# Kernel tuning notes

Hardware: AMD Instinct MI355X
Metric: run time of the kernel (lower is better)

Reference implementation:

```python
import jax, jax.numpy as jnp
import numpy as np

B, S, D = 8, 2048, 512
LN_EPS = 1e-5

def _layernorm(x, gamma, beta):
    mu = jnp.mean(x, axis=-1, keepdims=True)
    var = jnp.mean(jnp.square(x - mu), axis=-1, keepdims=True)
    return (x - mu) * jax.lax.rsqrt(var + LN_EPS) * gamma + beta

def setup_inputs() -> dict:
    key = jax.random.key(0)
    ks = jax.random.split(key, 10)
    s_in = 1.0 / np.sqrt(2 * D)
    s_d = 1.0 / np.sqrt(D)
    return {
        "Noise_x": jax.random.normal(ks[0], (B, S, D), jnp.float32),
        "X": jax.random.normal(ks[1], (B, S, D), jnp.float32),
        "cond": jax.random.normal(ks[2], (B, S, D), jnp.float32),
        "W_gate": jax.random.normal(ks[3], (2 * D, D), jnp.float32) * s_in,
        "b_gate": jnp.zeros((D,), jnp.float32),
        "W1": jax.random.normal(ks[4], (D, 2 * D), jnp.float32) * s_d,
        "b1": jnp.zeros((2 * D,), jnp.float32),
        "W2": jax.random.normal(ks[5], (2 * D, D), jnp.float32) * s_in,
        "b2": jnp.zeros((D,), jnp.float32),
        "g1": jnp.ones((D,), jnp.float32),
        "be1": jnp.zeros((D,), jnp.float32),
        "g2": jnp.ones((D,), jnp.float32),
        "be2": jnp.zeros((D,), jnp.float32),
    }

def reference(Noise_x, X, cond, W_gate, b_gate, W1, b1, W2, b2, g1, be1, g2, be2):
    # gated fusion of noise and condition
    combined = jnp.concatenate([Noise_x, cond], axis=-1)            # [B,S,2D]
    gate = jax.nn.sigmoid(combined @ W_gate + b_gate)               # [B,S,D]
    fused = gate * Noise_x + (1.0 - gate) * cond                    # [B,S,D]
    # hand-rolled attention: Q = fused, K = V = X
    scale = 1.0 / jnp.sqrt(jnp.asarray(D, fused.dtype))
    scores = jnp.einsum('bqd,bkd->bqk', fused, X) * scale           # [B,S,S]
    attn = jax.nn.softmax(scores, axis=-1)
    attn_out = jnp.einsum('bqk,bkd->bqd', attn, X)                  # [B,S,D]
    # residual + norm, FFN (exact GELU as in torch default), residual + norm
    q = _layernorm(fused + attn_out, g1, be1)
    ff = jax.nn.gelu(q @ W1 + b1, approximate=False) @ W2 + b2
    return _layernorm(q + ff, g2, be2)
```

## Files before the change

kernel.cpp:

```cpp
#include <hip/hip_runtime.h>
#include <math.h>

typedef unsigned short ushort_t;
typedef unsigned int uint_t;
typedef __attribute__((ext_vector_type(8))) short short8;
typedef __attribute__((ext_vector_type(4))) float floatx4;

constexpr int B = 8;
constexpr int S = 2048;
constexpr int D = 512;
constexpr int BS = B * S;
constexpr float LN_EPS = 1e-5f;
constexpr float ATTN_SCALE = 0.04419417382415922f;


__device__ __forceinline__ ushort_t f2bf(float f) {
    union { float f; uint_t u; } x; x.f = f;
    uint_t r = x.u + 0x7fffu + ((x.u >> 16) & 1u);
    return (ushort_t)(r >> 16);
}
__device__ __forceinline__ float bf2f(ushort_t h) {
    union { uint_t u; float f; } y; y.u = ((uint_t)h) << 16;
    return y.f;
}
__device__ __forceinline__ short8 pack8(float4 a, float4 b) {
    short8 p;
    p[0] = (short)f2bf(a.x); p[1] = (short)f2bf(a.y);
    p[2] = (short)f2bf(a.z); p[3] = (short)f2bf(a.w);
    p[4] = (short)f2bf(b.x); p[5] = (short)f2bf(b.y);
    p[6] = (short)f2bf(b.z); p[7] = (short)f2bf(b.w);
    return p;
}

__device__ __forceinline__ float blk_reduce_sum(float v, float* sm) {
#pragma unroll
    for (int o = 32; o; o >>= 1) v += __shfl_down(v, o, 64);
    __syncthreads();
    if ((threadIdx.x & 63) == 0) sm[threadIdx.x >> 6] = v;
    __syncthreads();
    return sm[0] + sm[1] + sm[2] + sm[3];
}
__device__ __forceinline__ float blk_reduce_max(float v, float* sm) {
#pragma unroll
    for (int o = 32; o; o >>= 1) v = fmaxf(v, __shfl_down(v, o, 64));
    __syncthreads();
    if ((threadIdx.x & 63) == 0) sm[threadIdx.x >> 6] = v;
    __syncthreads();
    return fmaxf(fmaxf(sm[0], sm[1]), fmaxf(sm[2], sm[3]));
}

__global__ __launch_bounds__(256) void transpose_cvt(
    const float* __restrict__ in, ushort_t* __restrict__ out, int R, int C) {
    __shared__ float tl[32][33];
    const size_t zoff = (size_t)blockIdx.z * R * C;
    const int tx = threadIdx.x & 31, ty = threadIdx.x >> 5;
    const int c0 = blockIdx.x * 32, r0 = blockIdx.y * 32;
#pragma unroll
    for (int i = 0; i < 4; i++)
        tl[ty + i * 8][tx] = in[zoff + (size_t)(r0 + ty + i * 8) * C + c0 + tx];
    __syncthreads();
#pragma unroll
    for (int i = 0; i < 4; i++)
        out[zoff + (size_t)(c0 + ty + i * 8) * R + r0 + tx] = f2bf(tl[tx][ty + i * 8]);
}

#define GEMM_PREAMBLE()                                                        \
    __shared__ ushort_t As[128 * 40];                                          \
    __shared__ ushort_t Bs[128 * 40];                                          \
    const int t = threadIdx.x;                                                 \
    const int m0 = blockIdx.y * 128, n0 = blockIdx.x * 128;                    \
    const int sr = t >> 2;                                          \
    const int sc = (t & 3) * 8;                                 \
    const int lane = t & 63, w = t >> 6;                                       \
    const int wm = (w >> 1) * 64, wn = (w & 1) * 64;                           \
    const int fr = lane & 15, fq = lane >> 4;                                  \
    floatx4 acc[4][4];                                                         \
    _Pragma("unroll") for (int i = 0; i < 4; i++)                              \
        _Pragma("unroll") for (int j = 0; j < 4; j++) {                        \
            acc[i][j][0] = 0.f; acc[i][j][1] = 0.f;                            \
            acc[i][j][2] = 0.f; acc[i][j][3] = 0.f; }

#define GEMM_MFMA_STAGE()                                                      \
    short8 af[4], bfg[4];                                                      \
    _Pragma("unroll") for (int i = 0; i < 4; i++) {                            \
        af[i]  = *(const short8*)&As[(wm + i * 16 + fr) * 40 + fq * 8];        \
        bfg[i] = *(const short8*)&Bs[(wn + i * 16 + fr) * 40 + fq * 8];        \
    }                                                                          \
    _Pragma("unroll") for (int i = 0; i < 4; i++)                              \
        _Pragma("unroll") for (int j = 0; j < 4; j++)                          \
            acc[i][j] = __builtin_amdgcn_mfma_f32_16x16x32_bf16(               \
                af[i], bfg[j], acc[i][j], 0, 0, 0);

__global__ __launch_bounds__(256) void gate_gemm(
    const float* __restrict__ NX, const float* __restrict__ CD,
    const ushort_t* __restrict__ WgT, const float* __restrict__ bg,
    ushort_t* __restrict__ Fb) {
    GEMM_PREAMBLE();
    const ushort_t* Bb = WgT + (size_t)n0 * 1024;

    for (int k0 = 0; k0 < 1024; k0 += 32) {
        const float* Asrc = (k0 < 512) ? NX : CD;
        const int kk = k0 & 511;
        const float* p0 = Asrc + (size_t)(m0 + sr) * 512 + kk + sc;
        const float* p1 = Asrc + (size_t)(m0 + sr + 64) * 512 + kk + sc;
        float4 f00 = *(const float4*)p0;       float4 f01 = *(const float4*)(p0 + 4);
        float4 f10 = *(const float4*)p1;       float4 f11 = *(const float4*)(p1 + 4);
        int4 b0 = *(const int4*)(Bb + (size_t)sr * 1024 + k0 + sc);
        int4 b1 = *(const int4*)(Bb + (size_t)(sr + 64) * 1024 + k0 + sc);
        short8 pa0 = pack8(f00, f01), pa1 = pack8(f10, f11);
        __syncthreads();
        *(short8*)&As[sr * 40 + sc] = pa0;
        *(short8*)&As[(sr + 64) * 40 + sc] = pa1;
        *(int4*)&Bs[sr * 40 + sc] = b0;
        *(int4*)&Bs[(sr + 64) * 40 + sc] = b1;
        __syncthreads();
        GEMM_MFMA_STAGE();
    }

#pragma unroll
    for (int i = 0; i < 4; i++) {
#pragma unroll
        for (int j = 0; j < 4; j++) {
#pragma unroll
            for (int r = 0; r < 4; r++) {
                const int m = m0 + wm + i * 16 + fq * 4 + r;
                const int n = n0 + wn + j * 16 + fr;
                const float z = acc[i][j][r] + bg[n];
                const float g = 1.f / (1.f + expf(-z));
                const size_t idx = (size_t)m * 512 + n;
                Fb[idx] = f2bf(g * NX[idx] + (1.f - g) * CD[idx]);
            }
        }
    }
}

#define GEMM3_PREAMBLE()                                                       \
    __shared__ ushort_t As[128 * 40];                                          \
    __shared__ ushort_t Bs[64 * 40];                                           \
    const int t = threadIdx.x;                                                 \
    const int m0 = blockIdx.y * 128, n0 = blockIdx.x * 64;                     \
    const int sr = t >> 2;                                          \
    const int sc = (t & 3) * 8;                                 \
    const int lane = t & 63, w = t >> 6;                                       \
    const int wm = w * 32;                                                     \
    const int fr = lane & 15, fq = lane >> 4;                                  \
    floatx4 acc[2][4];                                                         \
    _Pragma("unroll") for (int i = 0; i < 2; i++)                              \
        _Pragma("unroll") for (int j = 0; j < 4; j++) {                        \
            acc[i][j][0] = 0.f; acc[i][j][1] = 0.f;                            \
            acc[i][j][2] = 0.f; acc[i][j][3] = 0.f; }

#define GEMM3_MFMA_STAGE()                                                     \
    short8 af[2], bfg[4];                                                      \
    _Pragma("unroll") for (int i = 0; i < 2; i++)                              \
        af[i]  = *(const short8*)&As[(wm + i * 16 + fr) * 40 + fq * 8];        \
    _Pragma("unroll") for (int j = 0; j < 4; j++)                              \
        bfg[j] = *(const short8*)&Bs[(j * 16 + fr) * 40 + fq * 8];             \
    _Pragma("unroll") for (int i = 0; i < 2; i++)                              \
        _Pragma("unroll") for (int j = 0; j < 4; j++)                          \
            acc[i][j] = __builtin_amdgcn_mfma_f32_16x16x32_bf16(               \
                af[i], bfg[j], acc[i][j], 0, 0, 0);

template <int EPI>
__global__ __launch_bounds__(256) void gemm3_std(
    const ushort_t* __restrict__ A, int lda, long sAz,
    const ushort_t* __restrict__ Bt, int ldb, long sBz,
    void* __restrict__ Cv, int ldc, long sCz,
    int K, const float* __restrict__ bias, float scale, int init) {
    GEMM3_PREAMBLE();
    const ushort_t* Ab = A + (size_t)blockIdx.z * sAz + (size_t)m0 * lda;
    const ushort_t* Bb = Bt + (size_t)blockIdx.z * sBz + (size_t)n0 * ldb;

    for (int k0 = 0; k0 < K; k0 += 32) {
        int4 a0 = *(const int4*)(Ab + (size_t)sr * lda + k0 + sc);
        int4 a1 = *(const int4*)(Ab + (size_t)(sr + 64) * lda + k0 + sc);
        int4 b0 = *(const int4*)(Bb + (size_t)sr * ldb + k0 + sc);
        __syncthreads();
        *(int4*)&As[sr * 40 + sc] = a0;
        *(int4*)&As[(sr + 64) * 40 + sc] = a1;
        *(int4*)&Bs[sr * 40 + sc] = b0;
        __syncthreads();
        GEMM3_MFMA_STAGE();
    }

#pragma unroll
    for (int i = 0; i < 2; i++) {
#pragma unroll
        for (int j = 0; j < 4; j++) {
#pragma unroll
            for (int r = 0; r < 4; r++) {
                const int m = m0 + wm + i * 16 + fq * 4 + r;
                const int n = n0 + j * 16 + fr;
                float v = acc[i][j][r];
                if (EPI == 0) {
                    ushort_t* C = (ushort_t*)Cv + (size_t)blockIdx.z * sCz;
                    C[(size_t)m * ldc + n] = f2bf(v * scale);
                } else if (EPI == 1) {
                    const float x = v + bias[n];
                    const float gl = 0.5f * x * (1.f + erff(x * 0.70710678118654752f));
                    ushort_t* C = (ushort_t*)Cv;
                    C[(size_t)m * ldc + n] = f2bf(gl);
                } else {
                    float* T = (float*)Cv;
                    const size_t idx = (size_t)m * ldc + n;
                    T[idx] = T[idx] + v + (init ? bias[n] : 0.f);
                }
            }
        }
    }
}

__global__ __launch_bounds__(256) void qk_gemm3(
    const ushort_t* __restrict__ Qb, const float* __restrict__ Xf,
    ushort_t* __restrict__ Sc) {
    GEMM3_PREAMBLE();
    const ushort_t* Ab = Qb + (size_t)blockIdx.z * S * D + (size_t)m0 * D;
    const float*    Bf = Xf + (size_t)blockIdx.z * S * D + (size_t)n0 * D;
    ushort_t* Scb = Sc + (size_t)blockIdx.z * S * S;

    for (int k0 = 0; k0 < D; k0 += 32) {
        int4 a0 = *(const int4*)(Ab + (size_t)sr * D + k0 + sc);
        int4 a1 = *(const int4*)(Ab + (size_t)(sr + 64) * D + k0 + sc);
        const float* p0 = Bf + (size_t)sr * D + k0 + sc;
        float4 f00 = *(const float4*)p0;       float4 f01 = *(const float4*)(p0 + 4);
        short8 pb0 = pack8(f00, f01);
        __syncthreads();
        *(int4*)&As[sr * 40 + sc] = a0;
        *(int4*)&As[(sr + 64) * 40 + sc] = a1;
        *(short8*)&Bs[sr * 40 + sc] = pb0;
        __syncthreads();
        GEMM3_MFMA_STAGE();
    }

#pragma unroll
    for (int i = 0; i < 2; i++) {
#pragma unroll
        for (int j = 0; j < 4; j++) {
#pragma unroll
            for (int r = 0; r < 4; r++) {
                const int m = m0 + wm + i * 16 + fq * 4 + r;
                const int n = n0 + j * 16 + fr;
                Scb[(size_t)m * S + n] = f2bf(acc[i][j][r] * ATTN_SCALE);
            }
        }
    }
}

__global__ __launch_bounds__(256) void softmax_bf16(ushort_t* __restrict__ Sc) {
    __shared__ float sm[4];
    ushort_t* row = Sc + (size_t)blockIdx.x * 2048;
    const int t = threadIdx.x;
    ushort_t raw[8];
    *(int4*)raw = *(const int4*)(row + t * 8);
    float e[8];
    float mx = -1e30f;
#pragma unroll
    for (int j = 0; j < 8; j++) { e[j] = bf2f(raw[j]); mx = fmaxf(mx, e[j]); }
    mx = blk_reduce_max(mx, sm);
    float s = 0.f;
#pragma unroll
    for (int j = 0; j < 8; j++) { e[j] = expf(e[j] - mx); s += e[j]; }
    s = blk_reduce_sum(s, sm);
    const float inv = 1.f / s;
#pragma unroll
    for (int j = 0; j < 8; j++) raw[j] = f2bf(e[j] * inv);
    *(int4*)(row + t * 8) = *(const int4*)raw;
}

__global__ __launch_bounds__(256) void ln1_kernel(
    const ushort_t* __restrict__ Fb, const ushort_t* __restrict__ Ab,
    const float* __restrict__ g1, const float* __restrict__ be1,
    float* __restrict__ qf, ushort_t* __restrict__ qb) {
    __shared__ float sm[4];
    const size_t base = (size_t)blockIdx.x * 512;
    const int t = threadIdx.x;
    const float v0 = bf2f(Fb[base + t]) + bf2f(Ab[base + t]);
    const float v1 = bf2f(Fb[base + t + 256]) + bf2f(Ab[base + t + 256]);
    const float mu = blk_reduce_sum(v0 + v1, sm) * (1.f / 512.f);
    const float d0 = v0 - mu, d1 = v1 - mu;
    const float var = blk_reduce_sum(d0 * d0 + d1 * d1, sm) * (1.f / 512.f);
    const float rs = rsqrtf(var + LN_EPS);
    const float y0 = d0 * rs * g1[t] + be1[t];
    const float y1 = d1 * rs * g1[t + 256] + be1[t + 256];
    qf[base + t] = y0;          qf[base + t + 256] = y1;
    qb[base + t] = f2bf(y0);    qb[base + t + 256] = f2bf(y1);
}

__global__ __launch_bounds__(256) void ln2_kernel(
    float* __restrict__ T, const float* __restrict__ g,
    const float* __restrict__ be) {
    __shared__ float sm[4];
    const size_t base = (size_t)blockIdx.x * 512;
    const int t = threadIdx.x;
    const float v0 = T[base + t];
    const float v1 = T[base + t + 256];
    const float mu = blk_reduce_sum(v0 + v1, sm) * (1.f / 512.f);
    const float d0 = v0 - mu, d1 = v1 - mu;
    const float var = blk_reduce_sum(d0 * d0 + d1 * d1, sm) * (1.f / 512.f);
    const float rs = rsqrtf(var + LN_EPS);
    T[base + t] = d0 * rs * g[t] + be[t];
    T[base + t + 256] = d1 * rs * g[t + 256] + be[t + 256];
}

extern "C" void kernel_launch(void* const* d_in, const int* in_sizes, int n_in,
                              void* d_out, int out_size, void* d_ws, size_t ws_size,
                              hipStream_t stream) {
    const float* NX  = (const float*)d_in[0];
    const float* X   = (const float*)d_in[1];
    const float* CD  = (const float*)d_in[2];
    const float* Wg  = (const float*)d_in[3];
    const float* bg  = (const float*)d_in[4];
    const float* W1  = (const float*)d_in[5];
    const float* b1  = (const float*)d_in[6];
    const float* W2  = (const float*)d_in[7];
    const float* b2  = (const float*)d_in[8];
    const float* g1  = (const float*)d_in[9];
    const float* be1 = (const float*)d_in[10];
    const float* g2  = (const float*)d_in[11];
    const float* be2 = (const float*)d_in[12];

    ushort_t* slot0 = (ushort_t*)d_ws;
    ushort_t* slot1 = (ushort_t*)((char*)d_ws + 16777216);
    ushort_t* slot2 = (ushort_t*)((char*)d_ws + 33554432);
    ushort_t* attnb = slot0;
    ushort_t* hbuf  = slot0;
    ushort_t* Fb    = slot1;
    ushort_t* W1T   = slot1;
    ushort_t* W2T   = slot1 + 524288;
    ushort_t* WgT   = slot2;
    ushort_t* XbT   = slot2;
    ushort_t* qb    = slot2;
    ushort_t* Scb   = (ushort_t*)d_out;
    float*    qf    = (float*)d_out;

    transpose_cvt<<<dim3(512 / 32, 1024 / 32, 1), 256, 0, stream>>>(Wg, WgT, 1024, 512);

    gate_gemm<<<dim3(4, 128), 256, 0, stream>>>(NX, CD, WgT, bg, Fb);

    transpose_cvt<<<dim3(512 / 32, 2048 / 32, 8), 256, 0, stream>>>(X, XbT, 2048, 512);

    for (int g = 0; g < 2; g++) {
        const size_t go = (size_t)g * 4 * S * 512;
        qk_gemm3<<<dim3(32, 16, 4), 256, 0, stream>>>(Fb + go, X + go, Scb);
        softmax_bf16<<<4 * S, 256, 0, stream>>>(Scb);
        gemm3_std<0><<<dim3(8, 16, 4), 256, 0, stream>>>(
            Scb, S, (long)S * S,
            XbT + go, S, (long)D * S,
            (void*)(attnb + go), 512, (long)S * 512, S, nullptr, 1.f, 0);
    }

    ln1_kernel<<<BS, 256, 0, stream>>>(Fb, attnb, g1, be1, qf, qb);

    transpose_cvt<<<dim3(1024 / 32, 512 / 32, 1), 256, 0, stream>>>(W1, W1T, 512, 1024);
    transpose_cvt<<<dim3(512 / 32, 1024 / 32, 1), 256, 0, stream>>>(W2, W2T, 1024, 512);

    for (int h = 0; h < 2; h++) {
        gemm3_std<1><<<dim3(8, 128), 256, 0, stream>>>(
            qb, 512, 0, W1T + (size_t)h * 512 * 512, 512, 0,
            (void*)hbuf, 512, 0, 512, b1 + h * 512, 1.f, 0);
        gemm3_std<2><<<dim3(8, 128), 256, 0, stream>>>(
            hbuf, 512, 0, W2T + h * 512, 1024, 0,
            (void*)qf, 512, 0, 512, b2, 1.f, h == 0 ? 1 : 0);
    }

    ln2_kernel<<<BS, 256, 0, stream>>>(qf, g2, be2);
}
```

Measured before the change: 557.8 us.

## Prefetch next K-tile into registers during MFMA in all GEMM kernels

Each GEMM loop (generic, QK, gate) now loads the next K-slice from global memory into registers after the shared-memory store and before the MFMA stage, so global latency overlaps with compute. The gate GEMM also moves from a 128x128 tile to a 128x64 tile, doubling its grid. This is meant to hide global-load latency behind the MFMAs. In exchange it uses more live registers, and the smaller gate tile gives less data reuse per block.

Result: slower. 573.8 us (+2.9%).

```diff
diff --git a/kernel.cpp b/kernel.cpp
--- a/kernel.cpp
+++ b/kernel.cpp
@@ -62,76 +62,6 @@
 #pragma unroll
     for (int i = 0; i < 4; i++)
         out[zoff + (size_t)(c0 + ty + i * 8) * R + r0 + tx] = f2bf(tl[tx][ty + i * 8]);
-}
-
-#define GEMM_PREAMBLE()                                                        \
-    __shared__ ushort_t As[128 * 40];                                          \
-    __shared__ ushort_t Bs[128 * 40];                                          \
-    const int t = threadIdx.x;                                                 \
-    const int m0 = blockIdx.y * 128, n0 = blockIdx.x * 128;                    \
-    const int sr = t >> 2;                                          \
-    const int sc = (t & 3) * 8;                                 \
-    const int lane = t & 63, w = t >> 6;                                       \
-    const int wm = (w >> 1) * 64, wn = (w & 1) * 64;                           \
-    const int fr = lane & 15, fq = lane >> 4;                                  \
-    floatx4 acc[4][4];                                                         \
-    _Pragma("unroll") for (int i = 0; i < 4; i++)                              \
-        _Pragma("unroll") for (int j = 0; j < 4; j++) {                        \
-            acc[i][j][0] = 0.f; acc[i][j][1] = 0.f;                            \
-            acc[i][j][2] = 0.f; acc[i][j][3] = 0.f; }
-
-#define GEMM_MFMA_STAGE()                                                      \
-    short8 af[4], bfg[4];                                                      \
-    _Pragma("unroll") for (int i = 0; i < 4; i++) {                            \
-        af[i]  = *(const short8*)&As[(wm + i * 16 + fr) * 40 + fq * 8];        \
-        bfg[i] = *(const short8*)&Bs[(wn + i * 16 + fr) * 40 + fq * 8];        \
-    }                                                                          \
-    _Pragma("unroll") for (int i = 0; i < 4; i++)                              \
-        _Pragma("unroll") for (int j = 0; j < 4; j++)                          \
-            acc[i][j] = __builtin_amdgcn_mfma_f32_16x16x32_bf16(               \
-                af[i], bfg[j], acc[i][j], 0, 0, 0);
-
-__global__ __launch_bounds__(256) void gate_gemm(
-    const float* __restrict__ NX, const float* __restrict__ CD,
-    const ushort_t* __restrict__ WgT, const float* __restrict__ bg,
-    ushort_t* __restrict__ Fb) {
-    GEMM_PREAMBLE();
-    const ushort_t* Bb = WgT + (size_t)n0 * 1024;
-
-    for (int k0 = 0; k0 < 1024; k0 += 32) {
-        const float* Asrc = (k0 < 512) ? NX : CD;
-        const int kk = k0 & 511;
-        const float* p0 = Asrc + (size_t)(m0 + sr) * 512 + kk + sc;
-        const float* p1 = Asrc + (size_t)(m0 + sr + 64) * 512 + kk + sc;
-        float4 f00 = *(const float4*)p0;       float4 f01 = *(const float4*)(p0 + 4);
-        float4 f10 = *(const float4*)p1;       float4 f11 = *(const float4*)(p1 + 4);
-        int4 b0 = *(const int4*)(Bb + (size_t)sr * 1024 + k0 + sc);
-        int4 b1 = *(const int4*)(Bb + (size_t)(sr + 64) * 1024 + k0 + sc);
-        short8 pa0 = pack8(f00, f01), pa1 = pack8(f10, f11);
-        __syncthreads();
-        *(short8*)&As[sr * 40 + sc] = pa0;
-        *(short8*)&As[(sr + 64) * 40 + sc] = pa1;
-        *(int4*)&Bs[sr * 40 + sc] = b0;
-        *(int4*)&Bs[(sr + 64) * 40 + sc] = b1;
-        __syncthreads();
-        GEMM_MFMA_STAGE();
-    }
-
-#pragma unroll
-    for (int i = 0; i < 4; i++) {
-#pragma unroll
-        for (int j = 0; j < 4; j++) {
-#pragma unroll
-            for (int r = 0; r < 4; r++) {
-                const int m = m0 + wm + i * 16 + fq * 4 + r;
-                const int n = n0 + wn + j * 16 + fr;
-                const float z = acc[i][j][r] + bg[n];
-                const float g = 1.f / (1.f + expf(-z));
-                const size_t idx = (size_t)m * 512 + n;
-                Fb[idx] = f2bf(g * NX[idx] + (1.f - g) * CD[idx]);
-            }
-        }
-    }
 }
 
 #define GEMM3_PREAMBLE()                                                       \
@@ -151,18 +81,20 @@
             acc[i][j][2] = 0.f; acc[i][j][3] = 0.f; }
 
 #define GEMM3_MFMA_STAGE()                                                     \
-    short8 af[2], bfg[4];                                                      \
-    _Pragma("unroll") for (int i = 0; i < 2; i++)                              \
-        af[i]  = *(const short8*)&As[(wm + i * 16 + fr) * 40 + fq * 8];        \
-    _Pragma("unroll") for (int j = 0; j < 4; j++)                              \
-        bfg[j] = *(const short8*)&Bs[(j * 16 + fr) * 40 + fq * 8];             \
-    _Pragma("unroll") for (int i = 0; i < 2; i++)                              \
+    {                                                                          \
+        short8 af[2], bfg[4];                                                  \
+        _Pragma("unroll") for (int i = 0; i < 2; i++)                          \
+            af[i]  = *(const short8*)&As[(wm + i * 16 + fr) * 40 + fq * 8];    \
         _Pragma("unroll") for (int j = 0; j < 4; j++)                          \
-            acc[i][j] = __builtin_amdgcn_mfma_f32_16x16x32_bf16(               \
-                af[i], bfg[j], acc[i][j], 0, 0, 0);
+            bfg[j] = *(const short8*)&Bs[(j * 16 + fr) * 40 + fq * 8];         \
+        _Pragma("unroll") for (int i = 0; i < 2; i++)                          \
+            _Pragma("unroll") for (int j = 0; j < 4; j++)                      \
+                acc[i][j] = __builtin_amdgcn_mfma_f32_16x16x32_bf16(           \
+                    af[i], bfg[j], acc[i][j], 0, 0, 0);                        \
+    }
 
 template <int EPI>
-__global__ __launch_bounds__(256) void gemm3_std(
+__global__ __launch_bounds__(256) void gemm3p_std(
     const ushort_t* __restrict__ A, int lda, long sAz,
     const ushort_t* __restrict__ Bt, int ldb, long sBz,
     void* __restrict__ Cv, int ldc, long sCz,
@@ -171,15 +103,22 @@
     const ushort_t* Ab = A + (size_t)blockIdx.z * sAz + (size_t)m0 * lda;
     const ushort_t* Bb = Bt + (size_t)blockIdx.z * sBz + (size_t)n0 * ldb;
 
+    int4 ra0 = *(const int4*)(Ab + (size_t)sr * lda + sc);
+    int4 ra1 = *(const int4*)(Ab + (size_t)(sr + 64) * lda + sc);
+    int4 rb0 = *(const int4*)(Bb + (size_t)sr * ldb + sc);
+
     for (int k0 = 0; k0 < K; k0 += 32) {
-        int4 a0 = *(const int4*)(Ab + (size_t)sr * lda + k0 + sc);
-        int4 a1 = *(const int4*)(Ab + (size_t)(sr + 64) * lda + k0 + sc);
-        int4 b0 = *(const int4*)(Bb + (size_t)sr * ldb + k0 + sc);
-        __syncthreads();
-        *(int4*)&As[sr * 40 + sc] = a0;
-        *(int4*)&As[(sr + 64) * 40 + sc] = a1;
-        *(int4*)&Bs[sr * 40 + sc] = b0;
-        __syncthreads();
+        __syncthreads();
+        *(int4*)&As[sr * 40 + sc] = ra0;
+        *(int4*)&As[(sr + 64) * 40 + sc] = ra1;
+        *(int4*)&Bs[sr * 40 + sc] = rb0;
+        __syncthreads();
+        if (k0 + 32 < K) {
+            const int kn = k0 + 32 + sc;
+            ra0 = *(const int4*)(Ab + (size_t)sr * lda + kn);
+            ra1 = *(const int4*)(Ab + (size_t)(sr + 64) * lda + kn);
+            rb0 = *(const int4*)(Bb + (size_t)sr * ldb + kn);
+        }
         GEMM3_MFMA_STAGE();
     }
 
@@ -210,7 +149,56 @@
     }
 }
 
-__global__ __launch_bounds__(256) void qk_gemm3(
+__global__ __launch_bounds__(256) void gate_gemmp(
+    const float* __restrict__ NX, const float* __restrict__ CD,
+    const ushort_t* __restrict__ WgT, const float* __restrict__ bg,
+    ushort_t* __restrict__ Fb) {
+    GEMM3_PREAMBLE();
+    const ushort_t* Bb = WgT + (size_t)n0 * 1024;
+
+    float4 f00 = *(const float4*)(NX + (size_t)(m0 + sr) * 512 + sc);
+    float4 f01 = *(const float4*)(NX + (size_t)(m0 + sr) * 512 + sc + 4);
+    float4 f10 = *(const float4*)(NX + (size_t)(m0 + sr + 64) * 512 + sc);
+    float4 f11 = *(const float4*)(NX + (size_t)(m0 + sr + 64) * 512 + sc + 4);
+    int4 rb0 = *(const int4*)(Bb + (size_t)sr * 1024 + sc);
+
+    for (int k0 = 0; k0 < 1024; k0 += 32) {
+        __syncthreads();
+        *(short8*)&As[sr * 40 + sc] = pack8(f00, f01);
+        *(short8*)&As[(sr + 64) * 40 + sc] = pack8(f10, f11);
+        *(int4*)&Bs[sr * 40 + sc] = rb0;
+        __syncthreads();
+        if (k0 + 32 < 1024) {
+            const int k1 = k0 + 32;
+            const float* Asrc = (k1 < 512) ? NX : CD;
+            const int kk = (k1 & 511) + sc;
+            f00 = *(const float4*)(Asrc + (size_t)(m0 + sr) * 512 + kk);
+            f01 = *(const float4*)(Asrc + (size_t)(m0 + sr) * 512 + kk + 4);
+            f10 = *(const float4*)(Asrc + (size_t)(m0 + sr + 64) * 512 + kk);
+            f11 = *(const float4*)(Asrc + (size_t)(m0 + sr + 64) * 512 + kk + 4);
+            rb0 = *(const int4*)(Bb + (size_t)sr * 1024 + k1 + sc);
+        }
+        GEMM3_MFMA_STAGE();
+    }
+
+#pragma unroll
+    for (int i = 0; i < 2; i++) {
+#pragma unroll
+        for (int j = 0; j < 4; j++) {
+#pragma unroll
+            for (int r = 0; r < 4; r++) {
+                const int m = m0 + wm + i * 16 + fq * 4 + r;
+                const int n = n0 + j * 16 + fr;
+                const float z = acc[i][j][r] + bg[n];
+                const float g = 1.f / (1.f + expf(-z));
+                const size_t idx = (size_t)m * 512 + n;
+                Fb[idx] = f2bf(g * NX[idx] + (1.f - g) * CD[idx]);
+            }
+        }
+    }
+}
+
+__global__ __launch_bounds__(256) void qk_gemmp(
     const ushort_t* __restrict__ Qb, const float* __restrict__ Xf,
     ushort_t* __restrict__ Sc) {
     GEMM3_PREAMBLE();
@@ -218,17 +206,24 @@
     const float*    Bf = Xf + (size_t)blockIdx.z * S * D + (size_t)n0 * D;
     ushort_t* Scb = Sc + (size_t)blockIdx.z * S * S;
 
+    int4 ra0 = *(const int4*)(Ab + (size_t)sr * D + sc);
+    int4 ra1 = *(const int4*)(Ab + (size_t)(sr + 64) * D + sc);
+    float4 g0 = *(const float4*)(Bf + (size_t)sr * D + sc);
+    float4 g1 = *(const float4*)(Bf + (size_t)sr * D + sc + 4);
+
     for (int k0 = 0; k0 < D; k0 += 32) {
-        int4 a0 = *(const int4*)(Ab + (size_t)sr * D + k0 + sc);
-        int4 a1 = *(const int4*)(Ab + (size_t)(sr + 64) * D + k0 + sc);
-        const float* p0 = Bf + (size_t)sr * D + k0 + sc;
-        float4 f00 = *(const float4*)p0;       float4 f01 = *(const float4*)(p0 + 4);
-        short8 pb0 = pack8(f00, f01);
-        __syncthreads();
-        *(int4*)&As[sr * 40 + sc] = a0;
-        *(int4*)&As[(sr + 64) * 40 + sc] = a1;
-        *(short8*)&Bs[sr * 40 + sc] = pb0;
-        __syncthreads();
+        __syncthreads();
+        *(int4*)&As[sr * 40 + sc] = ra0;
+        *(int4*)&As[(sr + 64) * 40 + sc] = ra1;
+        *(short8*)&Bs[sr * 40 + sc] = pack8(g0, g1);
+        __syncthreads();
+        if (k0 + 32 < D) {
+            const int kn = k0 + 32 + sc;
+            ra0 = *(const int4*)(Ab + (size_t)sr * D + kn);
+            ra1 = *(const int4*)(Ab + (size_t)(sr + 64) * D + kn);
+            g0 = *(const float4*)(Bf + (size_t)sr * D + kn);
+            g1 = *(const float4*)(Bf + (size_t)sr * D + kn + 4);
+        }
         GEMM3_MFMA_STAGE();
     }
 
@@ -335,15 +330,15 @@
 
     transpose_cvt<<<dim3(512 / 32, 1024 / 32, 1), 256, 0, stream>>>(Wg, WgT, 1024, 512);
 
-    gate_gemm<<<dim3(4, 128), 256, 0, stream>>>(NX, CD, WgT, bg, Fb);
+    gate_gemmp<<<dim3(8, 128), 256, 0, stream>>>(NX, CD, WgT, bg, Fb);
 
     transpose_cvt<<<dim3(512 / 32, 2048 / 32, 8), 256, 0, stream>>>(X, XbT, 2048, 512);
 
     for (int g = 0; g < 2; g++) {
         const size_t go = (size_t)g * 4 * S * 512;
-        qk_gemm3<<<dim3(32, 16, 4), 256, 0, stream>>>(Fb + go, X + go, Scb);
+        qk_gemmp<<<dim3(32, 16, 4), 256, 0, stream>>>(Fb + go, X + go, Scb);
         softmax_bf16<<<4 * S, 256, 0, stream>>>(Scb);
-        gemm3_std<0><<<dim3(8, 16, 4), 256, 0, stream>>>(
+        gemm3p_std<0><<<dim3(8, 16, 4), 256, 0, stream>>>(
             Scb, S, (long)S * S,
             XbT + go, S, (long)D * S,
             (void*)(attnb + go), 512, (long)S * 512, S, nullptr, 1.f, 0);
@@ -355,10 +350,10 @@
     transpose_cvt<<<dim3(512 / 32, 1024 / 32, 1), 256, 0, stream>>>(W2, W2T, 1024, 512);
 
     for (int h = 0; h < 2; h++) {
-        gemm3_std<1><<<dim3(8, 128), 256, 0, stream>>>(
+        gemm3p_std<1><<<dim3(8, 128), 256, 0, stream>>>(
             qb, 512, 0, W1T + (size_t)h * 512 * 512, 512, 0,
             (void*)hbuf, 512, 0, 512, b1 + h * 512, 1.f, 0);
-        gemm3_std<2><<<dim3(8, 128), 256, 0, stream>>>(
+        gemm3p_std<2><<<dim3(8, 128), 256, 0, stream>>>(
             hbuf, 512, 0, W2T + h * 512, 1024, 0,
             (void*)qf, 512, 0, 512, b2, 1.f, h == 0 ? 1 : 0);
     }
```
